# Performance work log

Measured on AMD Instinct MI355X. Metric: run time of the kernel, lower is better.

## Reference

```python
import jax, jax.numpy as jnp
import numpy as np

B, S, H = 2, 2048, 1024
NH, HD = 16, 64  # num heads, head dim
EPS = 1e-12


def setup_inputs() -> dict:
    key = jax.random.key(0)
    ks = jax.random.split(key, 10)
    sc = 1.0 / np.sqrt(H)
    return {
        "hidden_states": jax.random.normal(ks[0], (B, S, H), jnp.float32),
        "Wq": jax.random.normal(ks[1], (H, H), jnp.float32) * sc,
        "bq": jnp.zeros((H,), jnp.float32),
        "Wk": jax.random.normal(ks[2], (H, H), jnp.float32) * sc,
        "bk": jnp.zeros((H,), jnp.float32),
        "Wv": jax.random.normal(ks[3], (H, H), jnp.float32) * sc,
        "bv": jnp.zeros((H,), jnp.float32),
        "Wo": jax.random.normal(ks[4], (H, H), jnp.float32) * sc,
        "bo": jnp.zeros((H,), jnp.float32),
        "ln_g": jnp.ones((H,), jnp.float32),
        "ln_b": jnp.zeros((H,), jnp.float32),
    }


def reference(hidden_states, Wq, bq, Wk, bk, Wv, bv, Wo, bo, ln_g, ln_b):
    x = hidden_states  # [B,S,H]
    def split_heads(t):
        return t.reshape(B, S, NH, HD).transpose(0, 2, 1, 3)  # [B,NH,S,HD]
    q = split_heads(x @ Wq.T + bq)
    k = split_heads(x @ Wk.T + bk)
    v = split_heads(x @ Wv.T + bv)
    scores = jnp.einsum("bhqd,bhkd->bhqk", q, k) / np.sqrt(HD)
    causal = jnp.tril(jnp.ones((S, S), bool))  # [S,S]
    scores = jnp.where(causal[None, None], scores, -jnp.inf)
    probs = jax.nn.softmax(scores, axis=-1)
    ctx = jnp.einsum("bhqk,bhkd->bhqd", probs, v)
    ctx = ctx.transpose(0, 2, 1, 3).reshape(B, S, H)
    attn_out = ctx @ Wo.T + bo
    y = attn_out + x
    mu = jnp.mean(y, axis=-1, keepdims=True)
    var = jnp.mean((y - mu) ** 2, axis=-1, keepdims=True)
    return (y - mu) / jnp.sqrt(var + EPS) * ln_g + ln_b
```

## Files before the change

### kernel.cpp

```cpp
#include <hip/hip_runtime.h>

#define B_  2
#define S_  2048
#define H_  1024
#define NH_ 16
#define HD_ 64
#define M_  (B_*S_)

typedef __attribute__((ext_vector_type(8))) __bf16 bf16x8;
typedef __attribute__((ext_vector_type(4))) float  f32x4;
typedef __attribute__((ext_vector_type(8))) unsigned short us8;
typedef __attribute__((ext_vector_type(4))) float  fl4;

__device__ __forceinline__ unsigned short f2bf(float f) {
    unsigned int u = __float_as_uint(f);
    u += 0x7fffu + ((u >> 16) & 1u);
    return (unsigned short)(u >> 16);
}

__global__ __launch_bounds__(256) void cast_kernel(
    const float* __restrict__ x,
    const float* __restrict__ wq, const float* __restrict__ wk,
    const float* __restrict__ wv, const float* __restrict__ wo,
    unsigned short* __restrict__ xb, unsigned short* __restrict__ wb) {
    size_t t  = (size_t)blockIdx.x * 256 + threadIdx.x;
    size_t e0 = t * 4;
    const size_t XN = (size_t)M_ * H_;
    const float* src;
    unsigned short* dst;
    if (e0 < XN) { src = x + e0; dst = xb + e0; }
    else {
        size_t j = e0 - XN;
        int w = (int)(j >> 20);
        size_t off = j & ((1u << 20) - 1);
        const float* wp = (w == 0) ? wq : (w == 1) ? wk : (w == 2) ? wv : wo;
        src = wp + off; dst = wb + j;
    }
    fl4 v = *(const fl4*)src;
    ushort4 o;
    o.x = f2bf(v.x); o.y = f2bf(v.y); o.z = f2bf(v.z); o.w = f2bf(v.w);
    *(ushort4*)dst = o;
}

__global__ __launch_bounds__(512) void gemm_qkv(
    const unsigned short* __restrict__ xb, const unsigned short* __restrict__ wb,
    const float* __restrict__ bq, const float* __restrict__ bk,
    const float* __restrict__ bv,
    unsigned short* __restrict__ qb, unsigned short* __restrict__ kbuf,
    unsigned short* __restrict__ vT) {
    __shared__ __align__(16) unsigned short As[128 * 72];
    __shared__ __align__(16) unsigned short Bs[128 * 72];
    const int z = blockIdx.z;
    const unsigned short* W = wb + ((size_t)z << 20);
    const int m0 = blockIdx.x * 128, n0 = blockIdx.y * 128;
    const int t = threadIdx.x, lane = t & 63, w = t >> 6;
    const int wm = w >> 2, wn = w & 3;
    const int quad = lane >> 4, l16 = lane & 15;
    const int sr = t >> 2, sc = (t & 3) * 16;
    const unsigned short* ga = xb + (size_t)(m0 + sr) * H_ + sc;
    const unsigned short* gb = W  + (size_t)(n0 + sr) * H_ + sc;

    us8 a0 = *(const us8*)(ga),     a1 = *(const us8*)(ga + 8);
    us8 b0 = *(const us8*)(gb),     b1 = *(const us8*)(gb + 8);

    f32x4 acc[4][2] = {};
    for (int k0 = 0; k0 < H_; k0 += 64) {
        if (k0) __syncthreads();
        *(us8*)&As[sr * 72 + sc]     = a0;  *(us8*)&As[sr * 72 + sc + 8] = a1;
        *(us8*)&Bs[sr * 72 + sc]     = b0;  *(us8*)&Bs[sr * 72 + sc + 8] = b1;
        __syncthreads();
        if (k0 + 64 < H_) {
            ga += 64; gb += 64;
            a0 = *(const us8*)(ga);  a1 = *(const us8*)(ga + 8);
            b0 = *(const us8*)(gb);  b1 = *(const us8*)(gb + 8);
        }
#pragma unroll
        for (int kk = 0; kk < 64; kk += 32) {
            bf16x8 af[4], bfr[2];
#pragma unroll
            for (int i = 0; i < 4; i++)
                af[i]  = *(const bf16x8*)&As[(wm * 64 + i * 16 + l16) * 72 + kk + quad * 8];
#pragma unroll
            for (int jn = 0; jn < 2; jn++)
                bfr[jn] = *(const bf16x8*)&Bs[(wn * 32 + jn * 16 + l16) * 72 + kk + quad * 8];
#pragma unroll
            for (int mi = 0; mi < 4; mi++)
#pragma unroll
                for (int ni = 0; ni < 2; ni++)
                    acc[mi][ni] = __builtin_amdgcn_mfma_f32_16x16x32_bf16(
                        af[mi], bfr[ni], acc[mi][ni], 0, 0, 0);
        }
    }
    const float* bias = (z == 0) ? bq : (z == 1) ? bk : bv;
    if (z == 2) {
#pragma unroll
        for (int mi = 0; mi < 4; mi++) {
#pragma unroll
            for (int ni = 0; ni < 2; ni++) {
                int col  = n0 + wn * 32 + ni * 16 + l16;
                float bval = bias[col];
                int row0 = m0 + wm * 64 + mi * 16 + quad * 4;
                int bb = row0 >> 11, s0 = row0 & 2047;
                ushort4 pk;
                pk.x = f2bf(acc[mi][ni][0] + bval);
                pk.y = f2bf(acc[mi][ni][1] + bval);
                pk.z = f2bf(acc[mi][ni][2] + bval);
                pk.w = f2bf(acc[mi][ni][3] + bval);
                *(ushort4*)&vT[((size_t)bb * NH_ * HD_ + col) * S_ + s0] = pk;
            }
        }
    } else {
        unsigned short* out = (z == 0) ? qb : kbuf;
        const float qs = (z == 0) ? 0.18033688f : 1.0f;
#pragma unroll
        for (int mi = 0; mi < 4; mi++) {
#pragma unroll
            for (int ni = 0; ni < 2; ni++) {
                int col = n0 + wn * 32 + ni * 16 + l16;
                float bval = bias[col];
#pragma unroll
                for (int r = 0; r < 4; r++) {
                    int row = m0 + wm * 64 + mi * 16 + quad * 4 + r;
                    out[(size_t)row * H_ + col] = f2bf((acc[mi][ni][r] + bval) * qs);
                }
            }
        }
    }
}

__global__ __launch_bounds__(512) void gemm_out(
    const unsigned short* __restrict__ ctxb, const unsigned short* __restrict__ wob,
    const float* __restrict__ bo, const float* __restrict__ x,
    float* __restrict__ y) {
    __shared__ __align__(16) unsigned short As[128 * 72];
    __shared__ __align__(16) unsigned short Bs[128 * 72];
    const int m0 = blockIdx.x * 128, n0 = blockIdx.y * 128;
    const int t = threadIdx.x, lane = t & 63, w = t >> 6;
    const int wm = w >> 2, wn = w & 3;
    const int quad = lane >> 4, l16 = lane & 15;
    const int sr = t >> 2, sc = (t & 3) * 16;
    const unsigned short* ga = ctxb + (size_t)(m0 + sr) * H_ + sc;
    const unsigned short* gb = wob  + (size_t)(n0 + sr) * H_ + sc;

    us8 a0 = *(const us8*)(ga),     a1 = *(const us8*)(ga + 8);
    us8 b0 = *(const us8*)(gb),     b1 = *(const us8*)(gb + 8);

    f32x4 acc[4][2] = {};
    for (int k0 = 0; k0 < H_; k0 += 64) {
        if (k0) __syncthreads();
        *(us8*)&As[sr * 72 + sc]     = a0;  *(us8*)&As[sr * 72 + sc + 8] = a1;
        *(us8*)&Bs[sr * 72 + sc]     = b0;  *(us8*)&Bs[sr * 72 + sc + 8] = b1;
        __syncthreads();
        if (k0 + 64 < H_) {
            ga += 64; gb += 64;
            a0 = *(const us8*)(ga);  a1 = *(const us8*)(ga + 8);
            b0 = *(const us8*)(gb);  b1 = *(const us8*)(gb + 8);
        }
#pragma unroll
        for (int kk = 0; kk < 64; kk += 32) {
            bf16x8 af[4], bfr[2];
#pragma unroll
            for (int i = 0; i < 4; i++)
                af[i]  = *(const bf16x8*)&As[(wm * 64 + i * 16 + l16) * 72 + kk + quad * 8];
#pragma unroll
            for (int jn = 0; jn < 2; jn++)
                bfr[jn] = *(const bf16x8*)&Bs[(wn * 32 + jn * 16 + l16) * 72 + kk + quad * 8];
#pragma unroll
            for (int mi = 0; mi < 4; mi++)
#pragma unroll
                for (int ni = 0; ni < 2; ni++)
                    acc[mi][ni] = __builtin_amdgcn_mfma_f32_16x16x32_bf16(
                        af[mi], bfr[ni], acc[mi][ni], 0, 0, 0);
        }
    }
#pragma unroll
    for (int mi = 0; mi < 4; mi++) {
#pragma unroll
        for (int ni = 0; ni < 2; ni++) {
            int col = n0 + wn * 32 + ni * 16 + l16;
            float bval = bo[col];
#pragma unroll
            for (int r = 0; r < 4; r++) {
                size_t idx = (size_t)(m0 + wm * 64 + mi * 16 + quad * 4 + r) * H_ + col;
                y[idx] = acc[mi][ni][r] + bval + x[idx];
            }
        }
    }
}

__global__ __launch_bounds__(512, 2) void attn_kernel(
    const unsigned short* __restrict__ qb, const unsigned short* __restrict__ kb,
    const unsigned short* __restrict__ vT, unsigned short* __restrict__ ctxb) {
    __shared__ __align__(16) unsigned short Ks[2][128 * 72];
    __shared__ __align__(16) unsigned short Vt[2][64 * 136];
    __shared__ __align__(16) unsigned short Ps[128 * 136];
    const int flat = blockIdx.x;
    const int xcd = flat & 7, slot = flat >> 3;
    const int bh  = xcd * 4 + (slot >> 3);
    const int j   = slot & 7;
    const int b = bh >> 4, h = bh & 15;
    const int t = threadIdx.x, lane = t & 63, wid = t >> 6;
    const int quad = lane >> 4, l16 = lane & 15;
    const int skr = t >> 2, skc = (t & 3) * 16;
    const int svr = t >> 3, svc = (t & 7) * 16;
    const size_t headoff = (size_t)h * HD_;
    const unsigned short* vtb = vT + ((size_t)(b * NH_ + h) * HD_) * S_;
    const int qrow = wid * 16 + l16;

#pragma unroll
    for (int ph = 0; ph < 2; ph++) {
        const int p2 = ph ? (15 - j) : j;
        const int q0 = p2 * 128;
        const int nsteps = p2 + 1;

        const size_t qr = (size_t)(b * S_ + q0 + qrow);
        bf16x8 qva = *(const bf16x8*)(qb + qr * H_ + headoff + quad * 8);
        bf16x8 qvb = *(const bf16x8*)(qb + qr * H_ + headoff + 32 + quad * 8);

        float m1 = -1e30f, l1 = 0.f;
        f32x4 o1[4] = {};

        const unsigned short* kptr = kb  + (size_t)(b * S_ + skr) * H_ + headoff + skc;
        const unsigned short* vptr = vtb + (size_t)svr * S_ + svc;
        us8 nk0 = *(const us8*)kptr,  nk1 = *(const us8*)(kptr + 8);
        us8 nv0 = *(const us8*)vptr,  nv1 = *(const us8*)(vptr + 8);
        __syncthreads();
        *(us8*)&Ks[0][skr * 72 + skc]      = nk0;
        *(us8*)&Ks[0][skr * 72 + skc + 8]  = nk1;
        *(us8*)&Vt[0][svr * 136 + svc]     = nv0;
        *(us8*)&Vt[0][svr * 136 + svc + 8] = nv1;
        __syncthreads();

        for (int s = 0; s < nsteps; s++) {
            const int buf = s & 1;
            const bool pf = (s + 1 < nsteps);
            if (pf) {
                kptr += (size_t)128 * H_;
                vptr += 128;
                nk0 = *(const us8*)kptr;  nk1 = *(const us8*)(kptr + 8);
                nv0 = *(const us8*)vptr;  nv1 = *(const us8*)(vptr + 8);
            }
            f32x4 sacc[8] = {};
            __builtin_amdgcn_s_setprio(1);
#pragma unroll
            for (int kk = 0; kk < 64; kk += 32) {
                bf16x8 bqf = (kk == 0) ? qva : qvb;
#pragma unroll
                for (int nt = 0; nt < 8; nt++) {
                    bf16x8 ak = *(const bf16x8*)&Ks[buf][(nt * 16 + l16) * 72 + kk + quad * 8];
                    sacc[nt] = __builtin_amdgcn_mfma_f32_16x16x32_bf16(ak, bqf, sacc[nt], 0, 0, 0);
                }
            }
            __builtin_amdgcn_s_setprio(0);
            if (s == p2) {
#pragma unroll
                for (int nt = 0; nt < 8; nt++) {
#pragma unroll
                    for (int r = 0; r < 4; r++) {
                        int key = nt * 16 + quad * 4 + r;
                        if (key > qrow) sacc[nt][r] = -1e30f;
                    }
                }
            }
            float tm[8];
#pragma unroll
            for (int nt = 0; nt < 8; nt++)
                tm[nt] = fmaxf(fmaxf(sacc[nt][0], sacc[nt][1]), fmaxf(sacc[nt][2], sacc[nt][3]));
            float mx = fmaxf(fmaxf(fmaxf(tm[0], tm[1]), fmaxf(tm[2], tm[3])),
                             fmaxf(fmaxf(tm[4], tm[5]), fmaxf(tm[6], tm[7])));
            mx = fmaxf(mx, __shfl_xor(mx, 16));
            mx = fmaxf(mx, __shfl_xor(mx, 32));
            const bool skip = __all(mx <= m1 + 5.0f);
            float m_new = skip ? m1 : fmaxf(m1, mx);
            float ss = 0.f;
#pragma unroll
            for (int nt = 0; nt < 8; nt++) {
                ushort4 pk;
                float p0 = __builtin_amdgcn_exp2f(sacc[nt][0] - m_new);
                float p1 = __builtin_amdgcn_exp2f(sacc[nt][1] - m_new);
                float p2e = __builtin_amdgcn_exp2f(sacc[nt][2] - m_new);
                float p3 = __builtin_amdgcn_exp2f(sacc[nt][3] - m_new);
                ss += (p0 + p1) + (p2e + p3);
                pk.x = (unsigned short)(__float_as_uint(p0) >> 16);
                pk.y = (unsigned short)(__float_as_uint(p1) >> 16);
                pk.z = (unsigned short)(__float_as_uint(p2e) >> 16);
                pk.w = (unsigned short)(__float_as_uint(p3) >> 16);
                *(ushort4*)&Ps[(wid * 16 + l16) * 136 + nt * 16 + quad * 4] = pk;
            }
            ss += __shfl_xor(ss, 16);
            ss += __shfl_xor(ss, 32);
            if (skip) {
                l1 += ss;
            } else {
                float alpha = __builtin_amdgcn_exp2f(m1 - m_new);
                l1 = l1 * alpha + ss;
                m1 = m_new;
#pragma unroll
                for (int dt = 0; dt < 4; dt++)
#pragma unroll
                    for (int r = 0; r < 4; r++) o1[dt][r] *= alpha;
            }
            __builtin_amdgcn_s_setprio(1);
#pragma unroll
            for (int kk = 0; kk < 128; kk += 32) {
                bf16x8 pfr = *(const bf16x8*)&Ps[(wid * 16 + l16) * 136 + kk + quad * 8];
#pragma unroll
                for (int dt = 0; dt < 4; dt++) {
                    bf16x8 vf = *(const bf16x8*)&Vt[buf][(dt * 16 + l16) * 136 + kk + quad * 8];
                    o1[dt] = __builtin_amdgcn_mfma_f32_16x16x32_bf16(vf, pfr, o1[dt], 0, 0, 0);
                }
            }
            __builtin_amdgcn_s_setprio(0);
            if (pf) {
                *(us8*)&Ks[buf ^ 1][skr * 72 + skc]      = nk0;
                *(us8*)&Ks[buf ^ 1][skr * 72 + skc + 8]  = nk1;
                *(us8*)&Vt[buf ^ 1][svr * 136 + svc]     = nv0;
                *(us8*)&Vt[buf ^ 1][svr * 136 + svc + 8] = nv1;
                __syncthreads();
            }
        }
        {
            const float inv = 1.0f / l1;
            size_t row = (size_t)(b * S_ + q0 + qrow);
#pragma unroll
            for (int dt = 0; dt < 4; dt++) {
                ushort4 pk;
                pk.x = f2bf(o1[dt][0] * inv);
                pk.y = f2bf(o1[dt][1] * inv);
                pk.z = f2bf(o1[dt][2] * inv);
                pk.w = f2bf(o1[dt][3] * inv);
                *(ushort4*)&ctxb[row * H_ + headoff + dt * 16 + quad * 4] = pk;
            }
        }
    }
}

__global__ __launch_bounds__(256) void ln_kernel(
    const float* __restrict__ y, const float* __restrict__ g,
    const float* __restrict__ bta, float* __restrict__ out) {
    __shared__ float red[8];
    const int row = blockIdx.x, t = threadIdx.x;
    fl4 v = *(const fl4*)(y + (size_t)row * H_ + t * 4);
    float s  = v.x + v.y + v.z + v.w;
    float sq = v.x * v.x + v.y * v.y + v.z * v.z + v.w * v.w;
    for (int m = 1; m < 64; m <<= 1) { s += __shfl_xor(s, m); sq += __shfl_xor(sq, m); }
    const int wid = t >> 6, lane = t & 63;
    if (lane == 0) { red[wid * 2] = s; red[wid * 2 + 1] = sq; }
    __syncthreads();
    s  = red[0] + red[2] + red[4] + red[6];
    sq = red[1] + red[3] + red[5] + red[7];
    float mu   = s * (1.0f / H_);
    float var  = sq * (1.0f / H_) - mu * mu;
    float rstd = rsqrtf(fmaxf(var, 0.f) + 1e-12f);
    fl4 gg = *(const fl4*)(g + t * 4);
    fl4 bb = *(const fl4*)(bta + t * 4);
    fl4 o;
    o.x = (v.x - mu) * rstd * gg.x + bb.x;
    o.y = (v.y - mu) * rstd * gg.y + bb.y;
    o.z = (v.z - mu) * rstd * gg.z + bb.z;
    o.w = (v.w - mu) * rstd * gg.w + bb.w;
    *(fl4*)(out + (size_t)row * H_ + t * 4) = o;
}

extern "C" void kernel_launch(void* const* d_in, const int* in_sizes, int n_in,
                              void* d_out, int out_size, void* d_ws, size_t ws_size,
                              hipStream_t stream) {
    const float* x  = (const float*)d_in[0];
    const float* Wq = (const float*)d_in[1];
    const float* bq = (const float*)d_in[2];
    const float* Wk = (const float*)d_in[3];
    const float* bk = (const float*)d_in[4];
    const float* Wv = (const float*)d_in[5];
    const float* bv = (const float*)d_in[6];
    const float* Wo = (const float*)d_in[7];
    const float* bo = (const float*)d_in[8];
    const float* lg = (const float*)d_in[9];
    const float* lb = (const float*)d_in[10];
    float* out = (float*)d_out;

    const size_t MEG = 1024u * 1024u;
    unsigned short* ws16 = (unsigned short*)d_ws;
    unsigned short* xb   = ws16;
    unsigned short* wb   = ws16 + 4 * MEG;
    unsigned short* qb   = ws16 + 8 * MEG;
    unsigned short* kb   = ws16 + 12 * MEG;
    unsigned short* vT   = ws16 + 16 * MEG;
    unsigned short* ctxb = ws16 + 20 * MEG;
    float* y = (float*)(ws16 + 24 * MEG);

    cast_kernel<<<8192, 256, 0, stream>>>(x, Wq, Wk, Wv, Wo, xb, wb);
    gemm_qkv<<<dim3(32, 8, 3), 512, 0, stream>>>(xb, wb, bq, bk, bv, qb, kb, vT);
    attn_kernel<<<dim3(256), 512, 0, stream>>>(qb, kb, vT, ctxb);
    gemm_out<<<dim3(32, 8), 512, 0, stream>>>(ctxb, wb + 3 * MEG, bo, x, y);
    ln_kernel<<<4096, 256, 0, stream>>>(y, lg, lb, out);
}
```

Baseline: 191.3 us.

## Split attention query-tile pairs into separate blocks and shrink shared memory

Each attention block previously processed two causal query tiles in sequence. Now the grid is doubled so each block handles one tile, with a remapped balanced tile order. LDS padding is reduced and the P staging buffer shrinks to a 32-column slice that is rewritten per k-chunk, so launch bounds can request 4 blocks per CU for higher occupancy. The trade-off is more LDS write/read traffic for P inside the PV loop, plus tighter register limits that may cause spills; the tighter padding may also add bank conflicts.

```diff
diff --git a/kernel.cpp b/kernel.cpp
--- a/kernel.cpp
+++ b/kernel.cpp
@@ -188,16 +188,20 @@
     }
 }
 
-__global__ __launch_bounds__(512, 2) void attn_kernel(
+__global__ __launch_bounds__(512, 4) void attn_kernel(
     const unsigned short* __restrict__ qb, const unsigned short* __restrict__ kb,
     const unsigned short* __restrict__ vT, unsigned short* __restrict__ ctxb) {
-    __shared__ __align__(16) unsigned short Ks[2][128 * 72];
-    __shared__ __align__(16) unsigned short Vt[2][64 * 136];
-    __shared__ __align__(16) unsigned short Ps[128 * 136];
+    __shared__ __align__(16) unsigned short Ks[2][128 * 68];
+    __shared__ __align__(16) unsigned short Vt[2][64 * 132];
+    __shared__ __align__(16) unsigned short Ps[128 * 44];
     const int flat = blockIdx.x;
-    const int xcd = flat & 7, slot = flat >> 3;
-    const int bh  = xcd * 4 + (slot >> 3);
-    const int j   = slot & 7;
+    const int rnd  = flat >> 8;
+    const int within = flat & 255;
+    const int xcd = within & 7, s2 = within >> 3;
+    const int bh  = xcd * 4 + (s2 >> 3);
+    const int j   = s2 & 7;
+    const int fj  = (j & 1) ? (15 - j) : j;
+    const int p2  = rnd ? (15 - fj) : fj;
     const int b = bh >> 4, h = bh & 15;
     const int t = threadIdx.x, lane = t & 63, wid = t >> 6;
     const int quad = lane >> 4, l16 = lane & 15;
@@ -207,130 +211,127 @@
     const unsigned short* vtb = vT + ((size_t)(b * NH_ + h) * HD_) * S_;
     const int qrow = wid * 16 + l16;
 
-#pragma unroll
-    for (int ph = 0; ph < 2; ph++) {
-        const int p2 = ph ? (15 - j) : j;
-        const int q0 = p2 * 128;
-        const int nsteps = p2 + 1;
-
-        const size_t qr = (size_t)(b * S_ + q0 + qrow);
-        bf16x8 qva = *(const bf16x8*)(qb + qr * H_ + headoff + quad * 8);
-        bf16x8 qvb = *(const bf16x8*)(qb + qr * H_ + headoff + 32 + quad * 8);
-
-        float m1 = -1e30f, l1 = 0.f;
-        f32x4 o1[4] = {};
-
-        const unsigned short* kptr = kb  + (size_t)(b * S_ + skr) * H_ + headoff + skc;
-        const unsigned short* vptr = vtb + (size_t)svr * S_ + svc;
-        us8 nk0 = *(const us8*)kptr,  nk1 = *(const us8*)(kptr + 8);
-        us8 nv0 = *(const us8*)vptr,  nv1 = *(const us8*)(vptr + 8);
-        __syncthreads();
-        *(us8*)&Ks[0][skr * 72 + skc]      = nk0;
-        *(us8*)&Ks[0][skr * 72 + skc + 8]  = nk1;
-        *(us8*)&Vt[0][svr * 136 + svc]     = nv0;
-        *(us8*)&Vt[0][svr * 136 + svc + 8] = nv1;
-        __syncthreads();
-
-        for (int s = 0; s < nsteps; s++) {
-            const int buf = s & 1;
-            const bool pf = (s + 1 < nsteps);
-            if (pf) {
-                kptr += (size_t)128 * H_;
-                vptr += 128;
-                nk0 = *(const us8*)kptr;  nk1 = *(const us8*)(kptr + 8);
-                nv0 = *(const us8*)vptr;  nv1 = *(const us8*)(vptr + 8);
-            }
-            f32x4 sacc[8] = {};
-            __builtin_amdgcn_s_setprio(1);
-#pragma unroll
-            for (int kk = 0; kk < 64; kk += 32) {
-                bf16x8 bqf = (kk == 0) ? qva : qvb;
-#pragma unroll
-                for (int nt = 0; nt < 8; nt++) {
-                    bf16x8 ak = *(const bf16x8*)&Ks[buf][(nt * 16 + l16) * 72 + kk + quad * 8];
-                    sacc[nt] = __builtin_amdgcn_mfma_f32_16x16x32_bf16(ak, bqf, sacc[nt], 0, 0, 0);
+    const int q0 = p2 * 128;
+    const int nsteps = p2 + 1;
+
+    const size_t qr = (size_t)(b * S_ + q0 + qrow);
+    bf16x8 qva = *(const bf16x8*)(qb + qr * H_ + headoff + quad * 8);
+    bf16x8 qvb = *(const bf16x8*)(qb + qr * H_ + headoff + 32 + quad * 8);
+
+    float m1 = -1e30f, l1 = 0.f;
+    f32x4 o1[4] = {};
+
+    const unsigned short* kptr = kb  + (size_t)(b * S_ + skr) * H_ + headoff + skc;
+    const unsigned short* vptr = vtb + (size_t)svr * S_ + svc;
+    us8 nk0 = *(const us8*)kptr,  nk1 = *(const us8*)(kptr + 8);
+    us8 nv0 = *(const us8*)vptr,  nv1 = *(const us8*)(vptr + 8);
+    *(us8*)&Ks[0][skr * 68 + skc]      = nk0;
+    *(us8*)&Ks[0][skr * 68 + skc + 8]  = nk1;
+    *(us8*)&Vt[0][svr * 132 + svc]     = nv0;
+    *(us8*)&Vt[0][svr * 132 + svc + 8] = nv1;
+    __syncthreads();
+
+    for (int s = 0; s < nsteps; s++) {
+        const int buf = s & 1;
+        const bool pf = (s + 1 < nsteps);
+        if (pf) {
+            kptr += (size_t)128 * H_;
+            vptr += 128;
+            nk0 = *(const us8*)kptr;  nk1 = *(const us8*)(kptr + 8);
+            nv0 = *(const us8*)vptr;  nv1 = *(const us8*)(vptr + 8);
+        }
+        f32x4 sacc[8] = {};
+        __builtin_amdgcn_s_setprio(1);
+#pragma unroll
+        for (int kk = 0; kk < 64; kk += 32) {
+            bf16x8 bqf = (kk == 0) ? qva : qvb;
+#pragma unroll
+            for (int nt = 0; nt < 8; nt++) {
+                bf16x8 ak = *(const bf16x8*)&Ks[buf][(nt * 16 + l16) * 68 + kk + quad * 8];
+                sacc[nt] = __builtin_amdgcn_mfma_f32_16x16x32_bf16(ak, bqf, sacc[nt], 0, 0, 0);
+            }
+        }
+        __builtin_amdgcn_s_setprio(0);
+        if (s == p2) {
+#pragma unroll
+            for (int nt = 0; nt < 8; nt++) {
+#pragma unroll
+                for (int r = 0; r < 4; r++) {
+                    int key = nt * 16 + quad * 4 + r;
+                    if (key > qrow) sacc[nt][r] = -1e30f;
                 }
             }
-            __builtin_amdgcn_s_setprio(0);
-            if (s == p2) {
-#pragma unroll
-                for (int nt = 0; nt < 8; nt++) {
-#pragma unroll
-                    for (int r = 0; r < 4; r++) {
-                        int key = nt * 16 + quad * 4 + r;
-                        if (key > qrow) sacc[nt][r] = -1e30f;
-                    }
-                }
-            }
-            float tm[8];
-#pragma unroll
-            for (int nt = 0; nt < 8; nt++)
-                tm[nt] = fmaxf(fmaxf(sacc[nt][0], sacc[nt][1]), fmaxf(sacc[nt][2], sacc[nt][3]));
-            float mx = fmaxf(fmaxf(fmaxf(tm[0], tm[1]), fmaxf(tm[2], tm[3])),
-                             fmaxf(fmaxf(tm[4], tm[5]), fmaxf(tm[6], tm[7])));
-            mx = fmaxf(mx, __shfl_xor(mx, 16));
-            mx = fmaxf(mx, __shfl_xor(mx, 32));
-            const bool skip = __all(mx <= m1 + 5.0f);
-            float m_new = skip ? m1 : fmaxf(m1, mx);
-            float ss = 0.f;
-#pragma unroll
-            for (int nt = 0; nt < 8; nt++) {
-                ushort4 pk;
-                float p0 = __builtin_amdgcn_exp2f(sacc[nt][0] - m_new);
-                float p1 = __builtin_amdgcn_exp2f(sacc[nt][1] - m_new);
-                float p2e = __builtin_amdgcn_exp2f(sacc[nt][2] - m_new);
-                float p3 = __builtin_amdgcn_exp2f(sacc[nt][3] - m_new);
-                ss += (p0 + p1) + (p2e + p3);
-                pk.x = (unsigned short)(__float_as_uint(p0) >> 16);
-                pk.y = (unsigned short)(__float_as_uint(p1) >> 16);
-                pk.z = (unsigned short)(__float_as_uint(p2e) >> 16);
-                pk.w = (unsigned short)(__float_as_uint(p3) >> 16);
-                *(ushort4*)&Ps[(wid * 16 + l16) * 136 + nt * 16 + quad * 4] = pk;
-            }
-            ss += __shfl_xor(ss, 16);
-            ss += __shfl_xor(ss, 32);
-            if (skip) {
-                l1 += ss;
-            } else {
-                float alpha = __builtin_amdgcn_exp2f(m1 - m_new);
-                l1 = l1 * alpha + ss;
-                m1 = m_new;
-#pragma unroll
-                for (int dt = 0; dt < 4; dt++)
-#pragma unroll
-                    for (int r = 0; r < 4; r++) o1[dt][r] *= alpha;
-            }
-            __builtin_amdgcn_s_setprio(1);
-#pragma unroll
-            for (int kk = 0; kk < 128; kk += 32) {
-                bf16x8 pfr = *(const bf16x8*)&Ps[(wid * 16 + l16) * 136 + kk + quad * 8];
-#pragma unroll
-                for (int dt = 0; dt < 4; dt++) {
-                    bf16x8 vf = *(const bf16x8*)&Vt[buf][(dt * 16 + l16) * 136 + kk + quad * 8];
-                    o1[dt] = __builtin_amdgcn_mfma_f32_16x16x32_bf16(vf, pfr, o1[dt], 0, 0, 0);
-                }
-            }
-            __builtin_amdgcn_s_setprio(0);
-            if (pf) {
-                *(us8*)&Ks[buf ^ 1][skr * 72 + skc]      = nk0;
-                *(us8*)&Ks[buf ^ 1][skr * 72 + skc + 8]  = nk1;
-                *(us8*)&Vt[buf ^ 1][svr * 136 + svc]     = nv0;
-                *(us8*)&Vt[buf ^ 1][svr * 136 + svc + 8] = nv1;
-                __syncthreads();
-            }
-        }
-        {
-            const float inv = 1.0f / l1;
-            size_t row = (size_t)(b * S_ + q0 + qrow);
+        }
+        float tm[8];
+#pragma unroll
+        for (int nt = 0; nt < 8; nt++)
+            tm[nt] = fmaxf(fmaxf(sacc[nt][0], sacc[nt][1]), fmaxf(sacc[nt][2], sacc[nt][3]));
+        float mx = fmaxf(fmaxf(fmaxf(tm[0], tm[1]), fmaxf(tm[2], tm[3])),
+                         fmaxf(fmaxf(tm[4], tm[5]), fmaxf(tm[6], tm[7])));
+        mx = fmaxf(mx, __shfl_xor(mx, 16));
+        mx = fmaxf(mx, __shfl_xor(mx, 32));
+        const bool skip = __all(mx <= m1 + 5.0f);
+        float m_new = skip ? m1 : fmaxf(m1, mx);
+        float ss = 0.f;
+        ushort4 pks[8];
+#pragma unroll
+        for (int nt = 0; nt < 8; nt++) {
+            float p0 = __builtin_amdgcn_exp2f(sacc[nt][0] - m_new);
+            float p1 = __builtin_amdgcn_exp2f(sacc[nt][1] - m_new);
+            float p2e = __builtin_amdgcn_exp2f(sacc[nt][2] - m_new);
+            float p3 = __builtin_amdgcn_exp2f(sacc[nt][3] - m_new);
+            ss += (p0 + p1) + (p2e + p3);
+            pks[nt].x = (unsigned short)(__float_as_uint(p0) >> 16);
+            pks[nt].y = (unsigned short)(__float_as_uint(p1) >> 16);
+            pks[nt].z = (unsigned short)(__float_as_uint(p2e) >> 16);
+            pks[nt].w = (unsigned short)(__float_as_uint(p3) >> 16);
+        }
+        ss += __shfl_xor(ss, 16);
+        ss += __shfl_xor(ss, 32);
+        if (skip) {
+            l1 += ss;
+        } else {
+            float alpha = __builtin_amdgcn_exp2f(m1 - m_new);
+            l1 = l1 * alpha + ss;
+            m1 = m_new;
+#pragma unroll
+            for (int dt = 0; dt < 4; dt++)
+#pragma unroll
+                for (int r = 0; r < 4; r++) o1[dt][r] *= alpha;
+        }
+        __builtin_amdgcn_s_setprio(1);
+#pragma unroll
+        for (int kk = 0; kk < 128; kk += 32) {
+            const int nb = kk >> 4;
+            *(ushort4*)&Ps[(wid * 16 + l16) * 44 + quad * 4]      = pks[nb];
+            *(ushort4*)&Ps[(wid * 16 + l16) * 44 + 16 + quad * 4] = pks[nb + 1];
+            bf16x8 pfr = *(const bf16x8*)&Ps[(wid * 16 + l16) * 44 + quad * 8];
 #pragma unroll
             for (int dt = 0; dt < 4; dt++) {
-                ushort4 pk;
-                pk.x = f2bf(o1[dt][0] * inv);
-                pk.y = f2bf(o1[dt][1] * inv);
-                pk.z = f2bf(o1[dt][2] * inv);
-                pk.w = f2bf(o1[dt][3] * inv);
-                *(ushort4*)&ctxb[row * H_ + headoff + dt * 16 + quad * 4] = pk;
-            }
+                bf16x8 vf = *(const bf16x8*)&Vt[buf][(dt * 16 + l16) * 132 + kk + quad * 8];
+                o1[dt] = __builtin_amdgcn_mfma_f32_16x16x32_bf16(vf, pfr, o1[dt], 0, 0, 0);
+            }
+        }
+        __builtin_amdgcn_s_setprio(0);
+        if (pf) {
+            *(us8*)&Ks[buf ^ 1][skr * 68 + skc]      = nk0;
+            *(us8*)&Ks[buf ^ 1][skr * 68 + skc + 8]  = nk1;
+            *(us8*)&Vt[buf ^ 1][svr * 132 + svc]     = nv0;
+            *(us8*)&Vt[buf ^ 1][svr * 132 + svc + 8] = nv1;
+            __syncthreads();
+        }
+    }
+    {
+        const float inv = 1.0f / l1;
+        size_t row = (size_t)(b * S_ + q0 + qrow);
+#pragma unroll
+        for (int dt = 0; dt < 4; dt++) {
+            ushort4 pk;
+            pk.x = f2bf(o1[dt][0] * inv);
+            pk.y = f2bf(o1[dt][1] * inv);
+            pk.z = f2bf(o1[dt][2] * inv);
+            pk.w = f2bf(o1[dt][3] * inv);
+            *(ushort4*)&ctxb[row * H_ + headoff + dt * 16 + quad * 4] = pk;
         }
     }
 }
@@ -390,7 +391,7 @@
 
     cast_kernel<<<8192, 256, 0, stream>>>(x, Wq, Wk, Wv, Wo, xb, wb);
     gemm_qkv<<<dim3(32, 8, 3), 512, 0, stream>>>(xb, wb, bq, bk, bv, qb, kb, vT);
-    attn_kernel<<<dim3(256), 512, 0, stream>>>(qb, kb, vT, ctxb);
+    attn_kernel<<<dim3(512), 512, 0, stream>>>(qb, kb, vT, ctxb);
     gemm_out<<<dim3(32, 8), 512, 0, stream>>>(ctxb, wb + 3 * MEG, bo, x, y);
     ln_kernel<<<4096, 256, 0, stream>>>(y, lg, lb, out);
 }
```

After: 190.4 us (median of 2 runs). No clear change (-0.5%).
